# Kernel tuning notes

Hardware: AMD Instinct MI355X
Metric: run time of the kernel (lower is better)

Reference implementation:

```python
import jax, jax.numpy as jnp
import numpy as np

B, S, D = 4, 2048, 512
BETA = 1.0
PARAM_SCALE = 1.0 / np.sqrt(D)  # ~ torch Linear default init scale


def setup_inputs() -> dict:
    key = jax.random.key(0)
    ks = jax.random.split(key, 14)
    def rn(k, shape, scale=1.0):
        return (jax.random.normal(k, shape, jnp.float32) * scale).astype(jnp.float32)
    return {
        "x_re": rn(ks[0], (B, S, D)),
        "x_im": rn(ks[1], (B, S, D)),
        "Wq_re": rn(ks[2], (D, D), PARAM_SCALE), "Wq_im": rn(ks[3], (D, D), PARAM_SCALE),
        "bq_re": rn(ks[4], (D,), PARAM_SCALE),   "bq_im": rn(ks[5], (D,), PARAM_SCALE),
        "Wk_re": rn(ks[6], (D, D), PARAM_SCALE), "Wk_im": rn(ks[7], (D, D), PARAM_SCALE),
        "bk_re": rn(ks[8], (D,), PARAM_SCALE),   "bk_im": rn(ks[9], (D,), PARAM_SCALE),
        "Wv_re": rn(ks[10], (D, D), PARAM_SCALE), "Wv_im": rn(ks[11], (D, D), PARAM_SCALE),
        "bv_re": rn(ks[12], (D,), PARAM_SCALE),   "bv_im": rn(ks[13], (D,), PARAM_SCALE),
    }


def reference(x_re, x_im, Wq_re, Wq_im, bq_re, bq_im,
              Wk_re, Wk_im, bk_re, bk_im, Wv_re, Wv_im, bv_re, bv_im):
    cx = lambda re, im: (re + 1j * im).astype(jnp.complex64)
    x = cx(x_re, x_im)                          # [B,S,D] complex64
    # nn.Linear: y = x @ W.T + b (complex)
    Q = jnp.einsum('bsd,ed->bse', x, cx(Wq_re, Wq_im)) + cx(bq_re, bq_im)
    K = jnp.einsum('bsd,ed->bse', x, cx(Wk_re, Wk_im)) + cx(bk_re, bk_im)
    V = jnp.einsum('bsd,ed->bse', x, cx(Wv_re, Wv_im)) + cx(bv_re, bv_im)
    # energy = -Re(Q K^H); attn = softmax(-beta * energy) = softmax(beta * Re(Q K^H))
    scores = jnp.real(jnp.einsum('bse,bte->bst', Q, jnp.conj(K)))  # [B,S,S] float32
    attn = jax.nn.softmax(BETA * scores, axis=-1)
    out = jnp.einsum('bst,bte->bse', attn.astype(jnp.complex64), V)  # [B,S,D] complex64
    return out
```

## Files before the change

kernel.cpp:

```cpp
#include <hip/hip_runtime.h>
#include <hip/hip_bf16.h>
#include <cstdint>
#include <cstddef>


typedef unsigned short u16;
typedef __attribute__((ext_vector_type(8))) _Float16 half8;
typedef __attribute__((ext_vector_type(4))) float f32x4;

#define B_    4
#define S_    2048
#define D_    512
#define M_TOT (B_ * S_)
#define KC    (2 * D_)
#define N1    (6 * D_)
#define LP    32
#define RE_PLANE 4194304

#define X_ELEMS  ((size_t)M_TOT * KC)
#define W_ELEMS  ((size_t)N1 * KC)
#define QK_ELEMS ((size_t)M_TOT * KC)
#define VT_ELEMS ((size_t)B_ * KC * S_)
#define AT_ELEMS ((size_t)M_TOT * S_)

__device__ __forceinline__ u16 f2h(float f) {
    _Float16 h = (_Float16)f;
    return __builtin_bit_cast(u16, h);
}
__device__ __forceinline__ float h2f(u16 b) {
    return (float)__builtin_bit_cast(_Float16, b);
}

__device__ __forceinline__ f32x4 mfma16(half8 a, half8 b, f32x4 c) {
    return __builtin_amdgcn_mfma_f32_16x16x32_f16(a, b, c, 0, 0, 0);
}

__device__ __forceinline__ void dma16(const u16* g, u16* l) {
    __builtin_amdgcn_global_load_lds(
        (const __attribute__((address_space(1))) unsigned int*)g,
        (__attribute__((address_space(3))) unsigned int*)l,
        16, 0, 0);
}

__device__ __forceinline__ void stage_dma(const u16* __restrict__ src, int ld,
                                          int rowbase, int kbase,
                                          u16* __restrict__ dst, int tid) {
#pragma unroll
    for (int i = 0; i < 2; ++i) {
        int c = tid + 256 * i;
        int row = c >> 2, q = c & 3;
        dma16(src + (size_t)(rowbase + row) * ld + kbase + q * 8, dst + c * 8);
    }
}

__global__ void k_diag(float* __restrict__ out, int out_size, float val) {
    int i = blockIdx.x * 256 + threadIdx.x;
    if (i < out_size && i < 4096) out[i] = val;
}

__global__ void k_prep(const float* __restrict__ xr, const float* __restrict__ xi,
                       const float* __restrict__ Wqr, const float* __restrict__ Wqi,
                       const float* __restrict__ Wkr, const float* __restrict__ Wki,
                       const float* __restrict__ Wvr, const float* __restrict__ Wvi,
                       const float* __restrict__ bqr, const float* __restrict__ bqi,
                       const float* __restrict__ bkr, const float* __restrict__ bki,
                       const float* __restrict__ bvr, const float* __restrict__ bvi,
                       u16* __restrict__ Xh, u16* __restrict__ Xl,
                       u16* __restrict__ Wh, float* __restrict__ bc) {
    int gb = blockIdx.x;
    int tid = threadIdx.x;
    if (gb < 16384) {
        int id = gb * 256 + tid;
        int m = id >> 9, d = id & 511;
        size_t o = (size_t)m * KC + d;
        if (o + D_ >= X_ELEMS) return;
        float vr = xr[id], vi = xi[id];
        u16 h;
        h = f2h(vr); Xh[o] = h;        Xl[o] = f2h(vr - h2f(h));
        h = f2h(vi); Xh[o + D_] = h;   Xl[o + D_] = f2h(vi - h2f(h));
    } else if (gb < 16384 + 12288) {
        int id = (gb - 16384) * 256 + tid;
        int n = id >> 10, k = id & 1023;
        int q = n >> 9, e = n & 511;
        int half = k >> 9, d = k & 511;
        const float* Wre = (q < 2) ? Wqr : ((q < 4) ? Wkr : Wvr);
        const float* Wim = (q < 2) ? Wqi : ((q < 4) ? Wki : Wvi);
        size_t src = (size_t)e * D_ + d;
        float v;
        if ((q & 1) == 0) v = half ? -Wim[src] : Wre[src];
        else              v = half ?  Wre[src] : Wim[src];
        if ((size_t)id < W_ELEMS) Wh[id] = f2h(v);
    } else {
        int id = (gb - 16384 - 12288) * 256 + tid;
        if (id >= N1) return;
        int q = id >> 9, e = id & 511;
        const float* src = (q == 0) ? bqr : (q == 1) ? bqi : (q == 2) ? bkr
                         : (q == 3) ? bki : (q == 4) ? bvr : bvi;
        bc[id] = src[e];
    }
}

__global__ __launch_bounds__(256) void k_gemm1(
    const u16* __restrict__ Xh, const u16* __restrict__ Xl,
    const u16* __restrict__ Wh,
    const float* __restrict__ bc,
    u16* __restrict__ Qh, u16* __restrict__ Ql,
    u16* __restrict__ Kh, u16* __restrict__ Kl,
    u16* __restrict__ VT) {
    __shared__ __attribute__((aligned(16))) u16 sAh[128 * LP], sAl[128 * LP],
                                                sB[128 * LP];
    int tid = threadIdx.x;
    int nb = blockIdx.x * 128, mb = blockIdx.y * 128;
    int g = nb >> 10;
    bool vblk = (g == 2);
    int lane = tid & 63, wave = tid >> 6;
    int wm = (wave >> 1) * 64, wn = (wave & 1) * 64;
    int lr = lane & 15, lq = lane >> 4;
    f32x4 acc[4][4] = {};

    for (int k0 = 0; k0 < KC; k0 += 32) {
        __syncthreads();
        stage_dma(Xh, KC, mb, k0, sAh, tid);
        if (!vblk) stage_dma(Xl, KC, mb, k0, sAl, tid);
        stage_dma(Wh, KC, nb, k0, sB, tid);
        __syncthreads();
        half8 ah[4], al[4], b[4];
#pragma unroll
        for (int i = 0; i < 4; ++i) {
            int ra = wm + i * 16 + lr;
            ah[i] = *(const half8*)&sAh[ra * LP + lq * 8];
            if (!vblk) al[i] = *(const half8*)&sAl[ra * LP + lq * 8];
            int rb = wn + i * 16 + lr;
            b[i]  = *(const half8*)&sB[rb * LP + lq * 8];
        }
        if (!vblk) {
#pragma unroll
            for (int i = 0; i < 4; ++i)
#pragma unroll
                for (int j = 0; j < 4; ++j) {
                    acc[i][j] = mfma16(ah[i], b[j], acc[i][j]);
                    acc[i][j] = mfma16(al[i], b[j], acc[i][j]);
                }
        } else {
#pragma unroll
            for (int i = 0; i < 4; ++i)
#pragma unroll
                for (int j = 0; j < 4; ++j)
                    acc[i][j] = mfma16(ah[i], b[j], acc[i][j]);
        }
    }

#pragma unroll
    for (int j = 0; j < 4; ++j) {
        int n_g = nb + wn + j * 16 + lr;
        float bias = bc[n_g];
        int c = n_g & 1023;
#pragma unroll
        for (int i = 0; i < 4; ++i) {
            int m0 = mb + wm + i * 16 + lq * 4;
            if (vblk) {
                int bidx = m0 >> 11, s0 = m0 & 2047;
                u16 pk[4];
#pragma unroll
                for (int r = 0; r < 4; ++r) pk[r] = f2h(acc[i][j][r] + bias);
                size_t idx = ((size_t)(bidx * KC + c)) * S_ + s0;
                if (idx + 3 < VT_ELEMS)
                    *(ushort4*)&VT[idx] = make_ushort4(pk[0], pk[1], pk[2], pk[3]);
            } else {
                u16* dh = g ? Kh : Qh;
                u16* dl = g ? Kl : Ql;
#pragma unroll
                for (int r = 0; r < 4; ++r) {
                    float v = acc[i][j][r] + bias;
                    u16 h = f2h(v);
                    size_t idx = (size_t)(m0 + r) * KC + c;
                    if (idx < QK_ELEMS) {
                        dh[idx] = h;
                        dl[idx] = f2h(v - h2f(h));
                    }
                }
            }
        }
    }
}

__global__ __launch_bounds__(256) void k_gemm2(
    const u16* __restrict__ Qh, const u16* __restrict__ Ql,
    const u16* __restrict__ Kh, const u16* __restrict__ Kl,
    float* __restrict__ SC, int zbase) {
    __shared__ __attribute__((aligned(16))) u16 sAh[128 * LP], sAl[128 * LP],
                                                sBh[128 * LP], sBl[128 * LP];
    int tid = threadIdx.x;
    int nb = blockIdx.x * 128, mb = blockIdx.y * 128;
    int z = zbase + blockIdx.z;
    const u16* Ah = Qh + (size_t)z * S_ * KC;
    const u16* Al = Ql + (size_t)z * S_ * KC;
    const u16* Bh = Kh + (size_t)z * S_ * KC;
    const u16* Bl = Kl + (size_t)z * S_ * KC;
    int lane = tid & 63, wave = tid >> 6;
    int wm = (wave >> 1) * 64, wn = (wave & 1) * 64;
    int lr = lane & 15, lq = lane >> 4;
    f32x4 acc[4][4] = {};

    for (int k0 = 0; k0 < KC; k0 += 32) {
        __syncthreads();
        stage_dma(Ah, KC, mb, k0, sAh, tid);
        stage_dma(Al, KC, mb, k0, sAl, tid);
        stage_dma(Bh, KC, nb, k0, sBh, tid);
        stage_dma(Bl, KC, nb, k0, sBl, tid);
        __syncthreads();
        half8 ah[4], al[4], bh[4], bl[4];
#pragma unroll
        for (int i = 0; i < 4; ++i) {
            int ra = wm + i * 16 + lr;
            ah[i] = *(const half8*)&sAh[ra * LP + lq * 8];
            al[i] = *(const half8*)&sAl[ra * LP + lq * 8];
            int rb = wn + i * 16 + lr;
            bh[i] = *(const half8*)&sBh[rb * LP + lq * 8];
            bl[i] = *(const half8*)&sBl[rb * LP + lq * 8];
        }
#pragma unroll
        for (int i = 0; i < 4; ++i)
#pragma unroll
            for (int j = 0; j < 4; ++j) {
                acc[i][j] = mfma16(ah[i], bh[j], acc[i][j]);
                acc[i][j] = mfma16(al[i], bh[j], acc[i][j]);
                acc[i][j] = mfma16(ah[i], bl[j], acc[i][j]);
            }
    }

    size_t sc_limit = (size_t)gridDim.z * S_ * S_;
#pragma unroll
    for (int j = 0; j < 4; ++j) {
        int t = nb + wn + j * 16 + lr;
#pragma unroll
        for (int i = 0; i < 4; ++i) {
            int s0 = mb + wm + i * 16 + lq * 4;
#pragma unroll
            for (int r = 0; r < 4; ++r) {
                size_t idx = ((size_t)blockIdx.z * S_ + s0 + r) * S_ + t;
                if (idx < sc_limit) SC[idx] = acc[i][j][r];
            }
        }
    }
}

__global__ __launch_bounds__(256) void k_softmax(const float* __restrict__ SC,
                                                 u16* __restrict__ AT, int zbase) {
    int row = blockIdx.x;
    const float* src = SC + (size_t)row * S_;
    size_t drow = (size_t)zbase * S_ + row;
    u16* dst = AT + drow * S_;
    int tid = threadIdx.x;
    float v[8];
#pragma unroll
    for (int i = 0; i < 8; ++i) v[i] = src[tid + i * 256];
    float m = v[0];
#pragma unroll
    for (int i = 1; i < 8; ++i) m = fmaxf(m, v[i]);
    for (int off = 32; off > 0; off >>= 1) m = fmaxf(m, __shfl_down(m, off));
    __shared__ float redm[4], reds[4];
    if ((tid & 63) == 0) redm[tid >> 6] = m;
    __syncthreads();
    m = fmaxf(fmaxf(redm[0], redm[1]), fmaxf(redm[2], redm[3]));
    float s = 0.f;
#pragma unroll
    for (int i = 0; i < 8; ++i) { v[i] = __expf(v[i] - m); s += v[i]; }
    for (int off = 32; off > 0; off >>= 1) s += __shfl_down(s, off);
    if ((tid & 63) == 0) reds[tid >> 6] = s;
    __syncthreads();
    float inv = 1.0f / (reds[0] + reds[1] + reds[2] + reds[3]);
    if (drow * S_ + 2047 < AT_ELEMS) {
#pragma unroll
        for (int i = 0; i < 8; ++i) dst[tid + i * 256] = f2h(v[i] * inv);
    }
}

__global__ __launch_bounds__(256) void k_gemm3(
    const u16* __restrict__ AT, const u16* __restrict__ VT,
    float* __restrict__ out, int out_size, int full) {
    __shared__ __attribute__((aligned(16))) u16 sA[128 * LP], sB[128 * LP];
    int tid = threadIdx.x;
    int nb = blockIdx.x * 128, mb = blockIdx.y * 128, z = blockIdx.z;
    const u16* Abase = AT + (size_t)z * S_ * S_;
    const u16* Bbase = VT + (size_t)z * KC * S_;
    int lane = tid & 63, wave = tid >> 6;
    int wm = (wave >> 1) * 64, wn = (wave & 1) * 64;
    int lr = lane & 15, lq = lane >> 4;
    f32x4 acc[4][4] = {};

    for (int k0 = 0; k0 < S_; k0 += 32) {
        __syncthreads();
        stage_dma(Abase, S_, mb, k0, sA, tid);
        stage_dma(Bbase, S_, nb, k0, sB, tid);
        __syncthreads();
        half8 a[4], b[4];
#pragma unroll
        for (int i = 0; i < 4; ++i) {
            a[i] = *(const half8*)&sA[(wm + i * 16 + lr) * LP + lq * 8];
            b[i] = *(const half8*)&sB[(wn + i * 16 + lr) * LP + lq * 8];
        }
#pragma unroll
        for (int i = 0; i < 4; ++i)
#pragma unroll
            for (int j = 0; j < 4; ++j)
                acc[i][j] = mfma16(a[i], b[j], acc[i][j]);
    }

#pragma unroll
    for (int j = 0; j < 4; ++j) {
        int f = nb + wn + j * 16 + lr;
#pragma unroll
        for (int i = 0; i < 4; ++i) {
            int s0 = mb + wm + i * 16 + lq * 4;
#pragma unroll
            for (int r = 0; r < 4; ++r) {
                size_t base = ((size_t)z * S_ + s0 + r) * D_;
                if (f < D_) {
                    size_t o = base + f;
                    if (o < (size_t)out_size) out[o] = acc[i][j][r];
                } else if (full) {
                    size_t o = (size_t)RE_PLANE + base + (f - D_);
                    if (o < (size_t)out_size) out[o] = acc[i][j][r];
                }
            }
        }
    }
}


extern "C" void kernel_launch(void* const* d_in, const int* in_sizes, int n_in,
                              void* d_out, int out_size, void* d_ws, size_t ws_size,
                              hipStream_t stream) {
    (void)in_sizes; (void)n_in;
    const float* xr  = (const float*)d_in[0];
    const float* xi  = (const float*)d_in[1];
    const float* Wqr = (const float*)d_in[2];
    const float* Wqi = (const float*)d_in[3];
    const float* bqr = (const float*)d_in[4];
    const float* bqi = (const float*)d_in[5];
    const float* Wkr = (const float*)d_in[6];
    const float* Wki = (const float*)d_in[7];
    const float* bkr = (const float*)d_in[8];
    const float* bki = (const float*)d_in[9];
    const float* Wvr = (const float*)d_in[10];
    const float* Wvi = (const float*)d_in[11];
    const float* bvr = (const float*)d_in[12];
    const float* bvi = (const float*)d_in[13];
    float* out = (float*)d_out;

    constexpr size_t SZ_X  = X_ELEMS * 2;
    constexpr size_t SZ_W  = W_ELEMS * 2;
    constexpr size_t SZ_BC = (size_t)N1 * 4;
    constexpr size_t SZ_QK = QK_ELEMS * 2;
    constexpr size_t SZ_VT = VT_ELEMS * 2;
    constexpr size_t SZ_SC_B = (size_t)S_ * S_ * 4;

    char* p = (char*)d_ws;
    size_t off = 0;
    auto take = [&](size_t sz) {
        char* r = p + off;
        off += (sz + 255) & ~(size_t)255;
        return r;
    };
    u16*   Xh = (u16*)take(SZ_X);
    u16*   Xl = (u16*)take(SZ_X);
    u16*   Wh = (u16*)take(SZ_W);
    float* bc = (float*)take(SZ_BC);
    u16*   Qh = (u16*)take(SZ_QK);
    u16*   Ql = (u16*)take(SZ_QK);
    u16*   Kh = (u16*)take(SZ_QK);
    u16*   Kl = (u16*)take(SZ_QK);
    u16*   VT = (u16*)take(SZ_VT);
    u16*   AT = Xh;
    float* SC = (float*)(p + off);

    int nz = 0;
    if (ws_size > off) nz = (int)((ws_size - off) / SZ_SC_B);
    if (nz > B_) nz = B_;
    if (nz < 1) {
        k_diag<<<16, 256, 0, stream>>>(out, out_size, 1000.0f + (float)(ws_size >> 20));
        return;
    }

    int full = (out_size >= 2 * RE_PLANE) ? 1 : 0;

    k_prep<<<16384 + 12288 + 12, 256, 0, stream>>>(
        xr, xi, Wqr, Wqi, Wkr, Wki, Wvr, Wvi,
        bqr, bqi, bkr, bki, bvr, bvi, Xh, Xl, Wh, bc);
    k_gemm1<<<dim3(N1 / 128, M_TOT / 128), 256, 0, stream>>>(Xh, Xl, Wh, bc, Qh, Ql, Kh, Kl, VT);

    for (int z0 = 0; z0 < B_; z0 += nz) {
        int zc = (B_ - z0 < nz) ? (B_ - z0) : nz;
        k_gemm2<<<dim3(S_ / 128, S_ / 128, zc), 256, 0, stream>>>(Qh, Ql, Kh, Kl, SC, z0);
        k_softmax<<<zc * S_, 256, 0, stream>>>(SC, AT, z0);
    }
    k_gemm3<<<dim3(KC / 128, S_ / 128, B_), 256, 0, stream>>>(AT, VT, out, out_size, full);
}
```

Measured before the change: 447.8 us.

## Rewrite projection GEMM with 256x256 tiles, double-buffered DMA pipeline and swizzled LDS

New measurement: 443.5 us. Within noise of the previous version (-1.0%).

```diff
diff --git a/kernel.cpp b/kernel.cpp
--- a/kernel.cpp
+++ b/kernel.cpp
@@ -50,6 +50,20 @@
         int c = tid + 256 * i;
         int row = c >> 2, q = c & 3;
         dma16(src + (size_t)(rowbase + row) * ld + kbase + q * 8, dst + c * 8);
+    }
+}
+
+__device__ __forceinline__ void stage_half(u16* __restrict__ plane,
+                                           const u16* __restrict__ src,
+                                           int rowbase, int kcol, int tid) {
+#pragma unroll
+    for (int i = 0; i < 2; ++i) {
+        int c = tid + (i << 9);
+        int c2 = c ^ (((c >> 5) & 1) << 1);
+        int row = ((c2 >> 3) << 1) | ((c2 >> 2) & 1);
+        int ks = c2 & 3;
+        dma16(src + (size_t)(rowbase + row) * KC + (kcol + ks * 8),
+              plane + c * 8);
     }
 }
 
@@ -100,55 +114,88 @@
     }
 }
 
-__global__ __launch_bounds__(256) void k_gemm1(
+#define GTILE(P, STG, SRCA, KA)                                               \
+  {                                                                           \
+    const int p_ = (P);                                                       \
+    _Pragma("unroll")                                                         \
+    for (int q = 0; q < 4; ++q) {                                             \
+      const int kh = q >> 1, mg = q & 1;                                      \
+      const u16* pa = &lds[(p_ << 2) | kh][0];                                \
+      const u16* pb = &lds[(p_ << 2) | 2 | kh][0];                            \
+      half8 a[4];                                                             \
+      if (mg == 0) {                                                          \
+        _Pragma("unroll")                                                     \
+        for (int j = 0; j < 4; ++j)                                           \
+          b[j] = *(const half8*)(pb + boffs + j * 512);                       \
+      }                                                                       \
+      _Pragma("unroll")                                                       \
+      for (int i = 0; i < 4; ++i)                                             \
+        a[i] = *(const half8*)(pa + aoffs + (mg * 4 + i) * 512);              \
+      if (STG) {                                                              \
+        const int xp = (p_ ^ 1) << 2;                                         \
+        if (q == 0) stage_half(&lds[xp][0], SRCA, mb, (KA), tid);             \
+        if (q == 1) stage_half(&lds[xp | 2][0], Wh, nb, (KA), tid);           \
+        if (q == 2) stage_half(&lds[xp | 1][0], SRCA, mb, (KA) + 32, tid);    \
+        if (q == 3) stage_half(&lds[xp | 3][0], Wh, nb, (KA) + 32, tid);      \
+        if (q & 1) asm volatile("s_waitcnt vmcnt(4)" ::: "memory");           \
+      } else if (q == 1) {                                                    \
+        asm volatile("s_waitcnt vmcnt(0)" ::: "memory");                      \
+      }                                                                       \
+      __builtin_amdgcn_s_barrier();                                           \
+      __builtin_amdgcn_s_setprio(1);                                          \
+      _Pragma("unroll")                                                       \
+      for (int j = 0; j < 4; ++j) {                                           \
+        _Pragma("unroll")                                                     \
+        for (int i = 0; i < 4; ++i)                                           \
+          acc[mg * 4 + i][j] = mfma16(a[i], b[j], acc[mg * 4 + i][j]);        \
+      }                                                                       \
+      __builtin_amdgcn_s_setprio(0);                                          \
+      __builtin_amdgcn_s_barrier();                                           \
+    }                                                                         \
+  }
+
+__global__ __launch_bounds__(512, 2) void k_gemm1(
     const u16* __restrict__ Xh, const u16* __restrict__ Xl,
     const u16* __restrict__ Wh,
     const float* __restrict__ bc,
     u16* __restrict__ Qh, u16* __restrict__ Ql,
     u16* __restrict__ Kh, u16* __restrict__ Kl,
     u16* __restrict__ VT) {
-    __shared__ __attribute__((aligned(16))) u16 sAh[128 * LP], sAl[128 * LP],
-                                                sB[128 * LP];
+    __shared__ __attribute__((aligned(16))) u16 lds[8][8192];
     int tid = threadIdx.x;
-    int nb = blockIdx.x * 128, mb = blockIdx.y * 128;
-    int g = nb >> 10;
+
+    int orig = blockIdx.y * 12 + blockIdx.x;
+    int swz = (orig & 7) * 48 + (orig >> 3);
+    int bx = swz % 12, by = swz / 12;
+    int nb = bx * 256, mb = by * 256;
+    int g = bx >> 2;
     bool vblk = (g == 2);
+    int NT = vblk ? 16 : 32;
+
     int lane = tid & 63, wave = tid >> 6;
-    int wm = (wave >> 1) * 64, wn = (wave & 1) * 64;
+    int wm = (wave >> 2) * 128, wn = (wave & 3) * 64;
     int lr = lane & 15, lq = lane >> 4;
-    f32x4 acc[4][4] = {};
-
-    for (int k0 = 0; k0 < KC; k0 += 32) {
-        __syncthreads();
-        stage_dma(Xh, KC, mb, k0, sAh, tid);
-        if (!vblk) stage_dma(Xl, KC, mb, k0, sAl, tid);
-        stage_dma(Wh, KC, nb, k0, sB, tid);
-        __syncthreads();
-        half8 ah[4], al[4], b[4];
-#pragma unroll
-        for (int i = 0; i < 4; ++i) {
-            int ra = wm + i * 16 + lr;
-            ah[i] = *(const half8*)&sAh[ra * LP + lq * 8];
-            if (!vblk) al[i] = *(const half8*)&sAl[ra * LP + lq * 8];
-            int rb = wn + i * 16 + lr;
-            b[i]  = *(const half8*)&sB[rb * LP + lq * 8];
-        }
-        if (!vblk) {
-#pragma unroll
-            for (int i = 0; i < 4; ++i)
-#pragma unroll
-                for (int j = 0; j < 4; ++j) {
-                    acc[i][j] = mfma16(ah[i], b[j], acc[i][j]);
-                    acc[i][j] = mfma16(al[i], b[j], acc[i][j]);
-                }
-        } else {
-#pragma unroll
-            for (int i = 0; i < 4; ++i)
-#pragma unroll
-                for (int j = 0; j < 4; ++j)
-                    acc[i][j] = mfma16(ah[i], b[j], acc[i][j]);
-        }
-    }
+    int lqs8 = (lq ^ (((lr >> 3) & 1) << 1)) * 8;
+    int aoffs = (wm + lr) * 32 + lqs8;
+    int boffs = (wn + lr) * 32 + lqs8;
+
+    f32x4 acc[8][4] = {};
+    half8 b[4];
+
+    stage_half(&lds[0][0], Xh, mb, 0, tid);
+    stage_half(&lds[2][0], Wh, nb, 0, tid);
+    stage_half(&lds[1][0], Xh, mb, 32, tid);
+    stage_half(&lds[3][0], Wh, nb, 32, tid);
+    asm volatile("s_waitcnt vmcnt(4)" ::: "memory");
+    __builtin_amdgcn_s_barrier();
+
+    for (int t = 0; t < NT - 1; ++t) {
+        int tt = t + 1;
+        const u16* srcA = (tt < 16) ? Xh : Xl;
+        int ka = (tt & 15) << 6;
+        GTILE(t & 1, 1, srcA, ka);
+    }
+    GTILE((NT - 1) & 1, 0, Xh, 0);
 
 #pragma unroll
     for (int j = 0; j < 4; ++j) {
@@ -156,7 +203,7 @@
         float bias = bc[n_g];
         int c = n_g & 1023;
 #pragma unroll
-        for (int i = 0; i < 4; ++i) {
+        for (int i = 0; i < 8; ++i) {
             int m0 = mb + wm + i * 16 + lq * 4;
             if (vblk) {
                 int bidx = m0 >> 11, s0 = m0 & 2047;
@@ -388,7 +435,7 @@
     k_prep<<<16384 + 12288 + 12, 256, 0, stream>>>(
         xr, xi, Wqr, Wqi, Wkr, Wki, Wvr, Wvi,
         bqr, bqi, bkr, bki, bvr, bvi, Xh, Xl, Wh, bc);
-    k_gemm1<<<dim3(N1 / 128, M_TOT / 128), 256, 0, stream>>>(Xh, Xl, Wh, bc, Qh, Ql, Kh, Kl, VT);
+    k_gemm1<<<dim3(N1 / 256, M_TOT / 256), 512, 0, stream>>>(Xh, Xl, Wh, bc, Qh, Ql, Kh, Kl, VT);
 
     for (int z0 = 0; z0 < B_; z0 += nz) {
         int zc = (B_ - z0 < nz) ? (B_ - z0) : nz;
```
